# Performance work log

Hardware: AMD Instinct MI355X
Metric: run time of the kernel (lower is better)

The kernel has to match this reference:

```python
import jax, jax.numpy as jnp
import numpy as np

B, N, H, HID, P = 4, 1024, 16, 64, 2


def setup_inputs() -> dict:
    key = jax.random.key(0)
    ks = jax.random.split(key, 8)
    positions = jax.random.normal(ks[0], (B, N, P), dtype=jnp.float32)
    key_padding_mask = jax.random.bernoulli(ks[1], 0.1, (B, N))
    # MLP params (Linear stores weight as (out,in) in torch; we keep (in,out) and matmul)
    s1 = 1.0 / np.sqrt(P)
    s2 = 1.0 / np.sqrt(HID)
    W1 = jax.random.uniform(ks[2], (P, HID), jnp.float32, -s1, s1)
    b1 = jax.random.uniform(ks[3], (HID,), jnp.float32, -s1, s1)
    W2 = jax.random.uniform(ks[4], (HID, HID), jnp.float32, -s2, s2)
    b2 = jax.random.uniform(ks[5], (HID,), jnp.float32, -s2, s2)
    W3 = jax.random.uniform(ks[6], (HID, H), jnp.float32, -s2, s2)
    b3 = jax.random.uniform(ks[7], (H,), jnp.float32, -s2, s2)
    return {"positions": positions, "key_padding_mask": key_padding_mask,
            "W1": W1, "b1": b1, "W2": W2, "b2": b2, "W3": W3, "b3": b3}


def reference(positions, key_padding_mask, W1, b1, W2, b2, W3, b3):
    # rel_pos[b, i, j] = pos[b, j] - pos[b, i]  -> (B, N, N, 2)
    rel = positions[:, None, :, :] - positions[:, :, None, :]
    h = jax.nn.relu(rel @ W1 + b1)          # (B, N, N, HID)
    h = jax.nn.relu(h @ W2 + b2)            # (B, N, N, HID)
    bias = h @ W3 + b3                      # (B, N, N, H)
    bias = jnp.transpose(bias, (0, 3, 1, 2))  # (B, H, N, N)
    # zero out rows/cols touching padded tokens
    combined = key_padding_mask[:, None, None, :] | key_padding_mask[:, None, :, None]
    bias = jnp.where(combined, 0.0, bias)
    return bias
```

## Files before the change

### kernel.cpp

```cpp
#include <hip/hip_runtime.h>
#include <hip/hip_bf16.h>
#include <hip/hip_fp16.h>

#define B_   4
#define N_   1024
#define H_   16
#define HID_ 64
#define TI   16
#define TJ   64
#define USJ  36
#define USO  68

typedef float    f32x4  __attribute__((ext_vector_type(4)));
typedef __fp16   fp16x2 __attribute__((ext_vector_type(2)));
typedef _Float16 f16x8  __attribute__((ext_vector_type(8)));
typedef unsigned int u32;

union F16x8U { u32 u[4]; f16x8 v; };

static __device__ __forceinline__ u32 pk(float a, float b) {
    union { fp16x2 f; u32 u; } r;
    r.f = __builtin_amdgcn_cvt_pkrtz(a, b);
    return r.u;
}
static __device__ __forceinline__ u32 pkadd_relu(u32 a, u32 b) {
    union { u32 u; fp16x2 f; } x, y, r;
    x.u = a; y.u = b;
    fp16x2 z = { (__fp16)0.f, (__fp16)0.f };
    fp16x2 s = x.f + y.f;
    r.f = __builtin_elementwise_max(s, z);
    return r.u;
}
static __device__ __forceinline__ u32 pkcvt_relu(float a, float b) {
    union { fp16x2 f; u32 u; } r;
    fp16x2 z = { (__fp16)0.f, (__fp16)0.f };
    fp16x2 s = __builtin_amdgcn_cvt_pkrtz(a, b);
    r.f = __builtin_elementwise_max(s, z);
    return r.u;
}

__global__ __launch_bounds__(256) void RelativePositionalBias_kernel(
    const float* __restrict__ pos,
    const int*   __restrict__ mask,
    const float* __restrict__ W1,
    const float* __restrict__ b1,
    const float* __restrict__ W2,
    const float* __restrict__ b2,
    const float* __restrict__ W3,
    const float* __restrict__ b3,
    float* __restrict__ out)
{
    __shared__ __align__(16) u32   ujL[TJ][USJ];
    __shared__ __align__(16) u32   uinL[TI][USJ];
    __shared__ __align__(16) float outb[2][2][H_][USO];

    const int b  = blockIdx.z;
    const int i0 = blockIdx.y * TI;
    const int j0 = blockIdx.x * TJ;
    const int tid = threadIdx.x;
    const int w = tid >> 6;
    const int l = tid & 63;
    const int g = l >> 4;
    const int c = l & 15;

    for (int it = tid; it < (TJ + TI) * 8; it += 256) {
        int r  = it >> 3;
        int qq = (it & 7) * 4;
        int k0 = qq * 2;
        int tok = (r < TJ) ? (j0 + r) : (i0 + (r - TJ));
        float2 p  = *(const float2*)&pos[(b * N_ + tok) * 2];
        float4 a0 = *(const float4*)&W1[k0];
        float4 a1 = *(const float4*)&W1[k0 + 4];
        float4 c0 = *(const float4*)&W1[HID_ + k0];
        float4 c1 = *(const float4*)&W1[HID_ + k0 + 4];
        float u0 = p.x*a0.x + p.y*c0.x, u1 = p.x*a0.y + p.y*c0.y;
        float u2 = p.x*a0.z + p.y*c0.z, u3 = p.x*a0.w + p.y*c0.w;
        float u4 = p.x*a1.x + p.y*c1.x, u5 = p.x*a1.y + p.y*c1.y;
        float u6 = p.x*a1.z + p.y*c1.z, u7 = p.x*a1.w + p.y*c1.w;
        uint4 o;
        if (r < TJ) {
            o.x = pk(u0, u1); o.y = pk(u2, u3); o.z = pk(u4, u5); o.w = pk(u6, u7);
            *(uint4*)&ujL[r][qq] = o;
        } else {
            float4 ba = *(const float4*)&b1[k0];
            float4 bb = *(const float4*)&b1[k0 + 4];
            o.x = pk(ba.x - u0, ba.y - u1); o.y = pk(ba.z - u2, ba.w - u3);
            o.z = pk(bb.x - u4, bb.y - u5); o.w = pk(bb.z - u6, bb.w - u7);
            *(uint4*)&uinL[r - TJ][qq] = o;
        }
    }

    F16x8U W2f[2][4];
    #pragma unroll
    for (int s = 0; s < 2; ++s)
        #pragma unroll
        for (int n = 0; n < 4; ++n)
            #pragma unroll
            for (int e = 0; e < 8; ++e)
                W2f[s][n].v[e] = (_Float16)W2[(32*s + 8*g + e) * HID_ + 16*n + c];

    F16x8U W3g[2];
    #pragma unroll
    for (int s = 0; s < 2; ++s)
        #pragma unroll
        for (int e = 0; e < 8; ++e)
            W3g[s].v[e] = (_Float16)W3[(32*s + 16*(e>>2) + 4*g + (e&3)) * H_ + c];

    f32x4 b2v[4];
    #pragma unroll
    for (int n = 0; n < 4; ++n)
        b2v[n] = *(const f32x4*)&b2[16*n + 4*g];

    const float b3v = b3[c];
    const int* maskb = &mask[b * N_ + i0];
    const int4 mjs = *(const int4*)&mask[b * N_ + j0 + 4*c];
    const size_t storeBase = ((size_t)(b*H_ + 4*w + g) << 20) + (size_t)(j0 + 4*c);

    __syncthreads();

    const uint4 pj0 = *(const uint4*)&ujL[16*w + c][4*g];
    const uint4 pj1 = *(const uint4*)&ujL[16*w + c][16 + 4*g];

    for (int t = 0; t < TI; t += 2) {
        const int p = (t >> 1) & 1;
        const int mi0 = maskb[t], mi1 = maskb[t + 1];

        #pragma unroll
        for (int rr = 0; rr < 2; ++rr) {
            if ((rr ? mi1 : mi0)) continue;
            const int tt = t + rr;

            uint4 uiA = *(const uint4*)&uinL[tt][4*g];
            uint4 uiB = *(const uint4*)&uinL[tt][16 + 4*g];

            F16x8U A1[2];
            A1[0].u[0] = pkadd_relu(pj0.x, uiA.x);
            A1[0].u[1] = pkadd_relu(pj0.y, uiA.y);
            A1[0].u[2] = pkadd_relu(pj0.z, uiA.z);
            A1[0].u[3] = pkadd_relu(pj0.w, uiA.w);
            A1[1].u[0] = pkadd_relu(pj1.x, uiB.x);
            A1[1].u[1] = pkadd_relu(pj1.y, uiB.y);
            A1[1].u[2] = pkadd_relu(pj1.z, uiB.z);
            A1[1].u[3] = pkadd_relu(pj1.w, uiB.w);

            f32x4 acc[4];
            #pragma unroll
            for (int n = 0; n < 4; ++n) {
                acc[n] = __builtin_amdgcn_mfma_f32_16x16x32_f16(W2f[0][n].v, A1[0].v, b2v[n], 0, 0, 0);
                acc[n] = __builtin_amdgcn_mfma_f32_16x16x32_f16(W2f[1][n].v, A1[1].v, acc[n], 0, 0, 0);
            }

            F16x8U A3[2];
            #pragma unroll
            for (int s = 0; s < 2; ++s) {
                A3[s].u[0] = pkcvt_relu(acc[2*s][0],     acc[2*s][1]);
                A3[s].u[1] = pkcvt_relu(acc[2*s][2],     acc[2*s][3]);
                A3[s].u[2] = pkcvt_relu(acc[2*s + 1][0], acc[2*s + 1][1]);
                A3[s].u[3] = pkcvt_relu(acc[2*s + 1][2], acc[2*s + 1][3]);
            }

            f32x4 acc3 = { b3v, b3v, b3v, b3v };
            acc3 = __builtin_amdgcn_mfma_f32_16x16x32_f16(A3[0].v, W3g[0].v, acc3, 0, 0, 0);
            acc3 = __builtin_amdgcn_mfma_f32_16x16x32_f16(A3[1].v, W3g[1].v, acc3, 0, 0, 0);

            *(f32x4*)&outb[p][rr][c][16*w + 4*g] = acc3;
        }

        __syncthreads();

        #pragma unroll
        for (int rr = 0; rr < 2; ++rr) {
            const int tt = t + rr;
            float4 o;
            if ((rr ? mi1 : mi0)) {
                o.x = 0.f; o.y = 0.f; o.z = 0.f; o.w = 0.f;
            } else {
                float4 v = *(const float4*)&outb[p][rr][4*w + g][4*c];
                o.x = mjs.x ? 0.f : v.x;
                o.y = mjs.y ? 0.f : v.y;
                o.z = mjs.z ? 0.f : v.z;
                o.w = mjs.w ? 0.f : v.w;
            }
            *(float4*)&out[storeBase + ((size_t)(i0 + tt) << 10)] = o;
        }
    }
}

extern "C" void kernel_launch(void* const* d_in, const int* in_sizes, int n_in,
                              void* d_out, int out_size, void* d_ws, size_t ws_size,
                              hipStream_t stream) {
    const float* pos  = (const float*)d_in[0];
    const int*   mask = (const int*)d_in[1];
    const float* W1   = (const float*)d_in[2];
    const float* b1   = (const float*)d_in[3];
    const float* W2   = (const float*)d_in[4];
    const float* b2   = (const float*)d_in[5];
    const float* W3   = (const float*)d_in[6];
    const float* b3   = (const float*)d_in[7];
    float* out = (float*)d_out;

    dim3 grid(N_ / TJ, N_ / TI, B_);
    RelativePositionalBias_kernel<<<grid, dim3(256), 0, stream>>>(
        pos, mask, W1, b1, W2, b2, W3, b3, out);
}
```

Baseline: 70.24 us.

## Store MFMA results directly to global, dropping LDS staging and barriers

```diff
diff --git a/kernel.cpp b/kernel.cpp
--- a/kernel.cpp
+++ b/kernel.cpp
@@ -6,10 +6,9 @@
 #define N_   1024
 #define H_   16
 #define HID_ 64
-#define TI   16
+#define TI   32
 #define TJ   64
 #define USJ  36
-#define USO  68
 
 typedef float    f32x4  __attribute__((ext_vector_type(4)));
 typedef __fp16   fp16x2 __attribute__((ext_vector_type(2)));
@@ -50,9 +49,8 @@
     const float* __restrict__ b3,
     float* __restrict__ out)
 {
-    __shared__ __align__(16) u32   ujL[TJ][USJ];
-    __shared__ __align__(16) u32   uinL[TI][USJ];
-    __shared__ __align__(16) float outb[2][2][H_][USO];
+    __shared__ __align__(16) u32 ujL[TJ][USJ];
+    __shared__ __align__(16) u32 uinL[TI][USJ];
 
     const int b  = blockIdx.z;
     const int i0 = blockIdx.y * TI;
@@ -113,25 +111,23 @@
 
     const float b3v = b3[c];
     const int* maskb = &mask[b * N_ + i0];
-    const int4 mjs = *(const int4*)&mask[b * N_ + j0 + 4*c];
-    const size_t storeBase = ((size_t)(b*H_ + 4*w + g) << 20) + (size_t)(j0 + 4*c);
+    const int4 mj = *(const int4*)&mask[b * N_ + j0 + 16*w + 4*g];
+    float* const outRow = out + ((size_t)(b*H_ + c) << 20) + (size_t)(j0 + 16*w + 4*g)
+                              + ((size_t)i0 << 10);
 
     __syncthreads();
 
     const uint4 pj0 = *(const uint4*)&ujL[16*w + c][4*g];
     const uint4 pj1 = *(const uint4*)&ujL[16*w + c][16 + 4*g];
 
-    for (int t = 0; t < TI; t += 2) {
-        const int p = (t >> 1) & 1;
-        const int mi0 = maskb[t], mi1 = maskb[t + 1];
+    #pragma unroll 4
+    for (int t = 0; t < TI; ++t) {
+        const int mi = maskb[t];
+        f32x4 o = { 0.f, 0.f, 0.f, 0.f };
 
-        #pragma unroll
-        for (int rr = 0; rr < 2; ++rr) {
-            if ((rr ? mi1 : mi0)) continue;
-            const int tt = t + rr;
-
-            uint4 uiA = *(const uint4*)&uinL[tt][4*g];
-            uint4 uiB = *(const uint4*)&uinL[tt][16 + 4*g];
+        if (!mi) {
+            uint4 uiA = *(const uint4*)&uinL[t][4*g];
+            uint4 uiB = *(const uint4*)&uinL[t][16 + 4*g];
 
             F16x8U A1[2];
             A1[0].u[0] = pkadd_relu(pj0.x, uiA.x);
@@ -163,26 +159,13 @@
             acc3 = __builtin_amdgcn_mfma_f32_16x16x32_f16(A3[0].v, W3g[0].v, acc3, 0, 0, 0);
             acc3 = __builtin_amdgcn_mfma_f32_16x16x32_f16(A3[1].v, W3g[1].v, acc3, 0, 0, 0);
 
-            *(f32x4*)&outb[p][rr][c][16*w + 4*g] = acc3;
+            o[0] = mj.x ? 0.f : acc3[0];
+            o[1] = mj.y ? 0.f : acc3[1];
+            o[2] = mj.z ? 0.f : acc3[2];
+            o[3] = mj.w ? 0.f : acc3[3];
         }
 
-        __syncthreads();
-
-        #pragma unroll
-        for (int rr = 0; rr < 2; ++rr) {
-            const int tt = t + rr;
-            float4 o;
-            if ((rr ? mi1 : mi0)) {
-                o.x = 0.f; o.y = 0.f; o.z = 0.f; o.w = 0.f;
-            } else {
-                float4 v = *(const float4*)&outb[p][rr][4*w + g][4*c];
-                o.x = mjs.x ? 0.f : v.x;
-                o.y = mjs.y ? 0.f : v.y;
-                o.z = mjs.z ? 0.f : v.z;
-                o.w = mjs.w ? 0.f : v.w;
-            }
-            *(float4*)&out[storeBase + ((size_t)(i0 + tt) << 10)] = o;
-        }
+        __builtin_nontemporal_store(o, (f32x4*)(outRow + ((size_t)t << 10)));
     }
 }
 
```

New measurement: 96.40 us. 37.2% more time.
